# Performance work log

Hardware: AMD Instinct MI355X
Metric: run time of the kernel (lower is better)

## Reference

```python
import jax, jax.numpy as jnp
import numpy as np

BN_EPS = 1e-5


def setup_inputs() -> dict:
    key = jax.random.key(0)
    ks = jax.random.split(key, 12)
    N, K, C_IN, C_OUT = 50000, 16, 128, 128
    C2 = 2 * C_OUT
    return {
        "features": jax.random.normal(ks[0], (N, C_IN), dtype=jnp.float32),
        "neighbor_idx": jax.random.randint(ks[1], (N, K), 0, N, dtype=jnp.int64),
        "W1": jax.random.normal(ks[2], (C_IN, C2), dtype=jnp.float32) * 0.05,
        "b1": jax.random.normal(ks[3], (C2,), dtype=jnp.float32) * 0.05,
        "gamma": jax.random.uniform(ks[4], (C2,), dtype=jnp.float32, minval=0.5, maxval=1.5),
        "beta": jax.random.normal(ks[5], (C2,), dtype=jnp.float32) * 0.05,
        "run_mean": jax.random.normal(ks[6], (C2,), dtype=jnp.float32) * 0.05,
        "run_var": jax.random.uniform(ks[7], (C2,), dtype=jnp.float32, minval=0.5, maxval=1.5),
        "Ws": jax.random.normal(ks[8], (C2, C2), dtype=jnp.float32) * 0.05,
        "Wm": jax.random.normal(ks[9], (C2, C_OUT), dtype=jnp.float32) * 0.05,
        "bm": jax.random.normal(ks[10], (C_OUT,), dtype=jnp.float32) * 0.05,
    }


def reference(features, neighbor_idx, W1, b1, gamma, beta, run_mean, run_var, Ws, Wm, bm):
    # mlp1: Linear + ReLU (no BN)
    x = jax.nn.relu(features @ W1 + b1)                     # (N, 2C)
    # gather_neighbour: irregular index_select
    g = x[neighbor_idx]                                     # (N, k, 2C)
    # BatchNorm1d over channel dim (inference semantics, running stats)
    inv = gamma * jax.lax.rsqrt(run_var + BN_EPS)
    g = (g - run_mean) * inv + beta                         # (N, k, 2C)
    # AttentivePooling: per-neighbor score linear (no bias), softmax over k
    scores = jax.nn.softmax(g @ Ws, axis=1)                 # (N, k, 2C)
    feat = jnp.sum(scores * g, axis=1)                      # (N, 2C)
    return feat @ Wm + bm                                   # (N, C_out)
```

## Files before the change

### kernel.cpp

```cpp
#include <hip/hip_runtime.h>
#include <cstddef>

#define C_IN  128
#define C2    256
#define C_OUT 128
#define KNBR  16
#define PTS   32

typedef unsigned short u16;
typedef __attribute__((ext_vector_type(8))) short bf16x8;
typedef __attribute__((ext_vector_type(8))) unsigned short u16x8;
typedef __attribute__((ext_vector_type(4))) float f32x4;

__device__ __forceinline__ float bf2f(u16 h) {
    return __uint_as_float(((unsigned int)h) << 16);
}
__device__ __forceinline__ u16 f2bf(float x) {
    unsigned int u = __float_as_uint(x);
    return (u16)((u + 0x7fffu + ((u >> 16) & 1u)) >> 16);
}

__global__ void prep_k(const float* __restrict__ W1, const float* __restrict__ Ws,
                       const float* __restrict__ Wm, const float* __restrict__ b1,
                       const float* __restrict__ gamma, const float* __restrict__ beta,
                       const float* __restrict__ mean, const float* __restrict__ var,
                       u16* __restrict__ W1t, u16* __restrict__ Wst,
                       u16* __restrict__ Wmt, float4* __restrict__ bnp)
{
    const int n = blockIdx.x, t = threadIdx.x;
    if (blockIdx.y == 0) {
        if (t < 128) W1t[n * 128 + t] = f2bf(W1[t * 256 + n]);
    } else if (blockIdx.y == 1) {
        Wst[n * 256 + t] = f2bf(Ws[t * 256 + n]);
    } else if (blockIdx.y == 2) {
        if (n < 128) Wmt[n * 256 + t] = f2bf(Wm[t * 128 + n]);
    } else if (n == 0) {
        float iv = gamma[t] * rsqrtf(var[t] + 1e-5f);
        bnp[t] = make_float4(b1[t], iv, beta[t] - mean[t] * iv, 0.f);
    }
}


__global__ __launch_bounds__(256, 3)
void mlp_k(const float* __restrict__ F, const u16* __restrict__ W1t,
           const u16* __restrict__ Wst, const float4* __restrict__ bnp,
           u16* __restrict__ packed, int N)
{
    __shared__ u16 xw[4][16][264];

    const int tid = threadIdx.x;
    const int w = tid >> 6, l = tid & 63, q = l >> 4, r = l & 15;
    const int m0 = blockIdx.x * 64 + w * 16;

    bf16x8 af[4];
    const int gr = m0 + r;
    #pragma unroll
    for (int t = 0; t < 4; t++) {
        float4 v0 = make_float4(0.f, 0.f, 0.f, 0.f), v1 = v0;
        if (gr < N) {
            const float* s = F + (size_t)gr * C_IN + t * 32 + q * 8;
            v0 = *(const float4*)s;
            v1 = *(const float4*)(s + 4);
        }
        bf16x8 a;
        a[0] = (short)f2bf(v0.x); a[1] = (short)f2bf(v0.y);
        a[2] = (short)f2bf(v0.z); a[3] = (short)f2bf(v0.w);
        a[4] = (short)f2bf(v1.x); a[5] = (short)f2bf(v1.y);
        a[6] = (short)f2bf(v1.z); a[7] = (short)f2bf(v1.w);
        af[t] = a;
    }

    {
        f32x4 acc[16];
        #pragma unroll
        for (int j = 0; j < 16; j++) acc[j] = (f32x4){0.f, 0.f, 0.f, 0.f};
        #pragma unroll
        for (int j = 0; j < 16; j++) {
            #pragma unroll
            for (int t = 0; t < 4; t++) {
                bf16x8 bf = *(const bf16x8*)(
                    W1t + (size_t)(j * 16 + r) * C_IN + t * 32 + q * 8);
                acc[j] = __builtin_amdgcn_mfma_f32_16x16x32_bf16(
                    af[t], bf, acc[j], 0, 0, 0);
            }
        }
        #pragma unroll
        for (int j = 0; j < 16; j++) {
            const float4 bp = bnp[j * 16 + r];
            #pragma unroll
            for (int p = 0; p < 4; p++) {
                float x = fmaxf(acc[j][p] + bp.x, 0.f) * bp.y + bp.z;
                xw[w][q * 4 + p][j * 16 + r] = f2bf(x);
            }
        }
    }
    asm volatile("s_waitcnt lgkmcnt(0)" ::: "memory");

    bf16x8 xa[8];
    #pragma unroll
    for (int t = 0; t < 8; t++)
        xa[t] = *(const bf16x8*)&xw[w][r][t * 32 + q * 8];

    f32x4 acc2[16];
    #pragma unroll
    for (int j = 0; j < 16; j++) acc2[j] = (f32x4){0.f, 0.f, 0.f, 0.f};
    #pragma unroll
    for (int j = 0; j < 16; j++) {
        #pragma unroll
        for (int t = 0; t < 8; t++) {
            bf16x8 bf = *(const bf16x8*)(
                Wst + (size_t)(j * 16 + r) * C2 + t * 32 + q * 8);
            acc2[j] = __builtin_amdgcn_mfma_f32_16x16x32_bf16(
                xa[t], bf, acc2[j], 0, 0, 0);
        }
    }

    #pragma unroll
    for (int j = 0; j < 16; j++) {
        #pragma unroll
        for (int p = 0; p < 4; p++) {
            const int gm = m0 + q * 4 + p;
            if (gm < N) {
                unsigned ey = f2bf(__expf(acc2[j][p]));
                unsigned xv = xw[w][q * 4 + p][j * 16 + r];
                *(unsigned*)(packed + (size_t)gm * 512 + (j * 16 + r) * 2) =
                    ey | (xv << 16);
            }
        }
    }
}

__global__ __launch_bounds__(256, 5)
void gather_out_k(const u16* __restrict__ packed, const int* __restrict__ nidx,
                  const u16* __restrict__ Bt, const float* __restrict__ bias,
                  float* __restrict__ Cf, int N)
{
    __shared__ int rows[PTS * KNBR];
    __shared__ __align__(16) u16 fsm[PTS * 264];

    const int tid = threadIdx.x;
    const int w = tid >> 6, l = tid & 63, q = l >> 4, r = l & 15;
    const int m0 = blockIdx.x * PTS;

    #pragma unroll
    for (int i = 0; i < 2; i++) {
        int idx = tid + i * 256;
        int n = m0 + (idx >> 4);
        rows[idx] = (n < N) ? nidx[n * KNBR + (idx & 15)] : 0;
    }
    __syncthreads();

    #pragma unroll 1
    for (int ip = 0; ip < 8; ip++) {
        const int pl = w * 8 + ip;
        float num[4] = {0.f, 0.f, 0.f, 0.f};
        float den[4] = {0.f, 0.f, 0.f, 0.f};
        #pragma unroll 1
        for (int hf = 0; hf < 2; hf++) {
            u16x8 v[8];
            #pragma unroll
            for (int k = 0; k < 8; k++)
                v[k] = *(const u16x8*)(packed +
                    (size_t)rows[pl * KNBR + hf * 8 + k] * 512 + l * 8);
            #pragma unroll
            for (int k = 0; k < 8; k++) {
                #pragma unroll
                for (int c = 0; c < 4; c++) {
                    float e = bf2f((u16)v[k][2 * c]);
                    float x = bf2f((u16)v[k][2 * c + 1]);
                    den[c] += e;
                    num[c] = fmaf(e, x, num[c]);
                }
            }
        }
        ushort4 o;
        o.x = f2bf(num[0] / den[0]); o.y = f2bf(num[1] / den[1]);
        o.z = f2bf(num[2] / den[2]); o.w = f2bf(num[3] / den[3]);
        *(ushort4*)&fsm[pl * 264 + l * 4] = o;
    }
    __syncthreads();

    const int wm = w & 1, wn = w >> 1;
    f32x4 acc[4] = {};

    #pragma unroll
    for (int k0 = 0; k0 < C2; k0 += 64) {
        #pragma unroll
        for (int h = 0; h < 2; h++) {
            bf16x8 af, bfr[4];
            af = *(const bf16x8*)&fsm[(wm * 16 + r) * 264 + k0 + h * 32 + q * 8];
            #pragma unroll
            for (int j = 0; j < 4; j++)
                bfr[j] = *(const bf16x8*)(Bt +
                    (size_t)(wn * 64 + j * 16 + r) * C2 + k0 + h * 32 + q * 8);
            #pragma unroll
            for (int j = 0; j < 4; j++)
                acc[j] = __builtin_amdgcn_mfma_f32_16x16x32_bf16(
                    af, bfr[j], acc[j], 0, 0, 0);
        }
    }
    __syncthreads();

    float* STF = (float*)fsm;
    #pragma unroll
    for (int j = 0; j < 4; j++) {
        const int ch = wn * 64 + j * 16 + r;
        const float bo = bias[ch];
        const int mb = wm * 16 + q * 4;
        #pragma unroll
        for (int p = 0; p < 4; p++)
            STF[(mb + p) * 132 + ch] = acc[j][p] + bo;
    }
    __syncthreads();
    #pragma unroll
    for (int i = 0; i < 4; i++) {
        int idx = tid + i * 256;
        int row = idx >> 5, c4 = (idx & 31) * 4;
        if (m0 + row < N)
            *(float4*)(Cf + (size_t)(m0 + row) * C_OUT + c4) =
                *(const float4*)&STF[row * 132 + c4];
    }
}

extern "C" void kernel_launch(void* const* d_in, const int* in_sizes, int n_in,
                              void* d_out, int out_size, void* d_ws, size_t ws_size,
                              hipStream_t stream)
{
    const float* features = (const float*)d_in[0];
    const int*   nidx     = (const int*)d_in[1];
    const float* W1       = (const float*)d_in[2];
    const float* b1       = (const float*)d_in[3];
    const float* gamma    = (const float*)d_in[4];
    const float* beta     = (const float*)d_in[5];
    const float* mean     = (const float*)d_in[6];
    const float* var      = (const float*)d_in[7];
    const float* Ws       = (const float*)d_in[8];
    const float* Wm       = (const float*)d_in[9];
    const float* bm       = (const float*)d_in[10];
    float* out = (float*)d_out;

    const int N = in_sizes[0] / C_IN;

    u16* packed = (u16*)d_ws;
    u16* W1t    = packed + (size_t)N * 512;
    u16* Wst    = W1t + 256 * 128;
    u16* Wmt    = Wst + 256 * 256;
    float4* bnp = (float4*)(Wmt + 128 * 256);

    prep_k<<<dim3(256, 4), 256, 0, stream>>>(W1, Ws, Wm, b1, gamma, beta,
                                             mean, var, W1t, Wst, Wmt, bnp);

    const int MT = (N + 63) / 64;
    const int GT = (N + PTS - 1) / PTS;

    mlp_k<<<MT, 256, 0, stream>>>(features, W1t, Wst, bnp, packed, N);
    gather_out_k<<<GT, 256, 0, stream>>>(packed, nidx, Wmt, bm, out, N);
}
```

Measured before the change: 304.5 us.

## Split fused MLP into two persistent kernels with LDS-resident weights

```diff
diff --git a/kernel.cpp b/kernel.cpp
--- a/kernel.cpp
+++ b/kernel.cpp
@@ -9,7 +9,6 @@
 
 typedef unsigned short u16;
 typedef __attribute__((ext_vector_type(8))) short bf16x8;
-typedef __attribute__((ext_vector_type(8))) unsigned short u16x8;
 typedef __attribute__((ext_vector_type(4))) float f32x4;
 
 __device__ __forceinline__ float bf2f(u16 h) {
@@ -41,90 +40,98 @@
 }
 
 
-__global__ __launch_bounds__(256, 3)
-void mlp_k(const float* __restrict__ F, const u16* __restrict__ W1t,
-           const u16* __restrict__ Wst, const float4* __restrict__ bnp,
-           u16* __restrict__ packed, int N)
-{
-    __shared__ u16 xw[4][16][264];
-
+__global__ __launch_bounds__(256)
+void mlp1_k(const float* __restrict__ F, const u16* __restrict__ W1t,
+            const float4* __restrict__ bnp, u16* __restrict__ packed, int N)
+{
+    __shared__ u16 Wl[256 * 136];
     const int tid = threadIdx.x;
     const int w = tid >> 6, l = tid & 63, q = l >> 4, r = l & 15;
-    const int m0 = blockIdx.x * 64 + w * 16;
-
-    bf16x8 af[4];
-    const int gr = m0 + r;
-    #pragma unroll
-    for (int t = 0; t < 4; t++) {
-        float4 v0 = make_float4(0.f, 0.f, 0.f, 0.f), v1 = v0;
-        if (gr < N) {
-            const float* s = F + (size_t)gr * C_IN + t * 32 + q * 8;
-            v0 = *(const float4*)s;
-            v1 = *(const float4*)(s + 4);
-        }
-        bf16x8 a;
-        a[0] = (short)f2bf(v0.x); a[1] = (short)f2bf(v0.y);
-        a[2] = (short)f2bf(v0.z); a[3] = (short)f2bf(v0.w);
-        a[4] = (short)f2bf(v1.x); a[5] = (short)f2bf(v1.y);
-        a[6] = (short)f2bf(v1.z); a[7] = (short)f2bf(v1.w);
-        af[t] = a;
-    }
-
-    {
-        f32x4 acc[16];
-        #pragma unroll
-        for (int j = 0; j < 16; j++) acc[j] = (f32x4){0.f, 0.f, 0.f, 0.f};
+
+    #pragma unroll
+    for (int i = 0; i < 16; i++) {
+        int idx = tid + i * 256;
+        int row = idx >> 4, g = (idx & 15) * 8;
+        *(uint4*)&Wl[row * 136 + g] = *(const uint4*)(W1t + row * 128 + g);
+    }
+    __syncthreads();
+
+    const int nwt = (N + 15) >> 4;
+    const int nw = gridDim.x * 4;
+    for (int wt = blockIdx.x * 4 + w; wt < nwt; wt += nw) {
+        const int base = wt * 16;
+        const int gr = min(base + r, N - 1);
+        bf16x8 af[4];
+        #pragma unroll
+        for (int kt = 0; kt < 4; kt++) {
+            const float* s = F + (size_t)gr * C_IN + kt * 32 + q * 8;
+            float4 v0 = *(const float4*)s;
+            float4 v1 = *(const float4*)(s + 4);
+            bf16x8 a;
+            a[0] = (short)f2bf(v0.x); a[1] = (short)f2bf(v0.y);
+            a[2] = (short)f2bf(v0.z); a[3] = (short)f2bf(v0.w);
+            a[4] = (short)f2bf(v1.x); a[5] = (short)f2bf(v1.y);
+            a[6] = (short)f2bf(v1.z); a[7] = (short)f2bf(v1.w);
+            af[kt] = a;
+        }
         #pragma unroll
         for (int j = 0; j < 16; j++) {
-            #pragma unroll
-            for (int t = 0; t < 4; t++) {
-                bf16x8 bf = *(const bf16x8*)(
-                    W1t + (size_t)(j * 16 + r) * C_IN + t * 32 + q * 8);
-                acc[j] = __builtin_amdgcn_mfma_f32_16x16x32_bf16(
-                    af[t], bf, acc[j], 0, 0, 0);
-            }
-        }
+            f32x4 acc = {0.f, 0.f, 0.f, 0.f};
+            #pragma unroll
+            for (int kt = 0; kt < 4; kt++) {
+                bf16x8 bf = *(const bf16x8*)&Wl[(j * 16 + r) * 136 + kt * 32 + q * 8];
+                acc = __builtin_amdgcn_mfma_f32_16x16x32_bf16(af[kt], bf, acc, 0, 0, 0);
+            }
+            const float4 bp = bnp[j * 16 + r];
+            #pragma unroll
+            for (int p = 0; p < 4; p++) {
+                const int gm = base + q * 4 + p;
+                if (gm < N) {
+                    float x = fmaxf(acc[p] + bp.x, 0.f) * bp.y + bp.z;
+                    packed[(size_t)gm * 512 + 256 + j * 16 + r] = f2bf(x);
+                }
+            }
+        }
+    }
+}
+
+__global__ __launch_bounds__(512)
+void mlp2_k(const u16* __restrict__ Wst, u16* __restrict__ packed, int N)
+{
+    __shared__ u16 Wsl[256 * 264];
+    const int tid = threadIdx.x;
+    const int w = tid >> 6, l = tid & 63, q = l >> 4, r = l & 15;
+
+    #pragma unroll
+    for (int i = 0; i < 16; i++) {
+        int idx = tid + i * 512;
+        int row = idx >> 5, g = (idx & 31) * 8;
+        *(uint4*)&Wsl[row * 264 + g] = *(const uint4*)(Wst + row * 256 + g);
+    }
+    __syncthreads();
+
+    const int nwt = (N + 15) >> 4;
+    const int nw = gridDim.x * 8;
+    for (int wt = blockIdx.x * 8 + w; wt < nwt; wt += nw) {
+        const int base = wt * 16;
+        const int gr = min(base + r, N - 1);
+        bf16x8 xa[8];
+        #pragma unroll
+        for (int kt = 0; kt < 8; kt++)
+            xa[kt] = *(const bf16x8*)(packed + (size_t)gr * 512 + 256 + kt * 32 + q * 8);
         #pragma unroll
         for (int j = 0; j < 16; j++) {
-            const float4 bp = bnp[j * 16 + r];
+            f32x4 acc = {0.f, 0.f, 0.f, 0.f};
+            #pragma unroll
+            for (int kt = 0; kt < 8; kt++) {
+                bf16x8 bf = *(const bf16x8*)&Wsl[(j * 16 + r) * 264 + kt * 32 + q * 8];
+                acc = __builtin_amdgcn_mfma_f32_16x16x32_bf16(xa[kt], bf, acc, 0, 0, 0);
+            }
             #pragma unroll
             for (int p = 0; p < 4; p++) {
-                float x = fmaxf(acc[j][p] + bp.x, 0.f) * bp.y + bp.z;
-                xw[w][q * 4 + p][j * 16 + r] = f2bf(x);
-            }
-        }
-    }
-    asm volatile("s_waitcnt lgkmcnt(0)" ::: "memory");
-
-    bf16x8 xa[8];
-    #pragma unroll
-    for (int t = 0; t < 8; t++)
-        xa[t] = *(const bf16x8*)&xw[w][r][t * 32 + q * 8];
-
-    f32x4 acc2[16];
-    #pragma unroll
-    for (int j = 0; j < 16; j++) acc2[j] = (f32x4){0.f, 0.f, 0.f, 0.f};
-    #pragma unroll
-    for (int j = 0; j < 16; j++) {
-        #pragma unroll
-        for (int t = 0; t < 8; t++) {
-            bf16x8 bf = *(const bf16x8*)(
-                Wst + (size_t)(j * 16 + r) * C2 + t * 32 + q * 8);
-            acc2[j] = __builtin_amdgcn_mfma_f32_16x16x32_bf16(
-                xa[t], bf, acc2[j], 0, 0, 0);
-        }
-    }
-
-    #pragma unroll
-    for (int j = 0; j < 16; j++) {
-        #pragma unroll
-        for (int p = 0; p < 4; p++) {
-            const int gm = m0 + q * 4 + p;
-            if (gm < N) {
-                unsigned ey = f2bf(__expf(acc2[j][p]));
-                unsigned xv = xw[w][q * 4 + p][j * 16 + r];
-                *(unsigned*)(packed + (size_t)gm * 512 + (j * 16 + r) * 2) =
-                    ey | (xv << 16);
+                const int gm = base + q * 4 + p;
+                if (gm < N)
+                    packed[(size_t)gm * 512 + j * 16 + r] = f2bf(__expf(acc[p]));
             }
         }
     }
@@ -157,20 +164,22 @@
         float den[4] = {0.f, 0.f, 0.f, 0.f};
         #pragma unroll 1
         for (int hf = 0; hf < 2; hf++) {
-            u16x8 v[8];
-            #pragma unroll
-            for (int k = 0; k < 8; k++)
-                v[k] = *(const u16x8*)(packed +
-                    (size_t)rows[pl * KNBR + hf * 8 + k] * 512 + l * 8);
+            ushort4 eh[8], xh[8];
             #pragma unroll
             for (int k = 0; k < 8; k++) {
-                #pragma unroll
-                for (int c = 0; c < 4; c++) {
-                    float e = bf2f((u16)v[k][2 * c]);
-                    float x = bf2f((u16)v[k][2 * c + 1]);
-                    den[c] += e;
-                    num[c] = fmaf(e, x, num[c]);
-                }
+                const size_t b = (size_t)rows[pl * KNBR + hf * 8 + k] * 512;
+                eh[k] = *(const ushort4*)(packed + b + l * 4);
+                xh[k] = *(const ushort4*)(packed + b + 256 + l * 4);
+            }
+            #pragma unroll
+            for (int k = 0; k < 8; k++) {
+                float e0 = bf2f(eh[k].x), e1 = bf2f(eh[k].y);
+                float e2 = bf2f(eh[k].z), e3 = bf2f(eh[k].w);
+                den[0] += e0; den[1] += e1; den[2] += e2; den[3] += e3;
+                num[0] = fmaf(e0, bf2f(xh[k].x), num[0]);
+                num[1] = fmaf(e1, bf2f(xh[k].y), num[1]);
+                num[2] = fmaf(e2, bf2f(xh[k].z), num[2]);
+                num[3] = fmaf(e3, bf2f(xh[k].w), num[3]);
             }
         }
         ushort4 o;
@@ -250,9 +259,9 @@
     prep_k<<<dim3(256, 4), 256, 0, stream>>>(W1, Ws, Wm, b1, gamma, beta,
                                              mean, var, W1t, Wst, Wmt, bnp);
 
-    const int MT = (N + 63) / 64;
     const int GT = (N + PTS - 1) / PTS;
 
-    mlp_k<<<MT, 256, 0, stream>>>(features, W1t, Wst, bnp, packed, N);
+    mlp1_k<<<512, 256, 0, stream>>>(features, W1t, bnp, packed, N);
+    mlp2_k<<<256, 512, 0, stream>>>(Wst, packed, N);
     gather_out_k<<<GT, 256, 0, stream>>>(packed, nidx, Wmt, bm, out, N);
 }
```

Measured after the change: 357.9 us. +17.5%, slower.
